# Kernel optimization log

Measured on AMD Instinct MI355X. Metric: run time of the kernel, lower is better.

The kernel has to match this reference:

```python
import jax, jax.numpy as jnp
import numpy as np

UNITS = 2048
D_IN = 96
BATCH = 64
T = 512
C_IN = 10        # connectivity_input: nnz per input-kernel row
C_REC = 10       # connectivity_recurrent: nnz per recurrent-kernel column
INPUT_SCALING = 1.0
SPECTRAL_RADIUS = 0.99
LEAKY = 1.0


def setup_inputs() -> dict:
    rng = np.random.default_rng(0)
    # --- input kernel: sparse (D_IN, UNITS), C_IN nonzeros per row (COO) ---
    krows = np.repeat(np.arange(D_IN), C_IN).astype(np.int32)                 # [D_IN*C_IN]
    kcols = np.stack([rng.choice(UNITS, size=C_IN, replace=False)
                      for _ in range(D_IN)]).reshape(-1).astype(np.int32)
    kvals = (2.0 * (2.0 * rng.random(D_IN * C_IN) - 1.0)).astype(np.float32) * np.float32(INPUT_SCALING)
    # --- recurrent kernel: sparse (UNITS, UNITS), C_REC nonzeros per column ---
    # rec_idx[i, j] = source row feeding output unit (column) i
    rec_idx = np.stack([rng.choice(UNITS, size=C_REC, replace=False)
                        for _ in range(UNITS)]).astype(np.int32)              # [UNITS, C_REC]
    rec_vals = (2.0 * (2.0 * rng.random((UNITS, C_REC)) - 1.0)).astype(np.float32)
    # spectral-radius normalization via exact eigenvalues (matches tf.linalg.eig path, leaky==1)
    W = np.zeros((UNITS, UNITS), np.float32)
    W[rec_idx.reshape(-1), np.repeat(np.arange(UNITS), C_REC)] = rec_vals.reshape(-1)
    rho = np.abs(np.linalg.eigvals(W)).max()
    rec_vals = rec_vals * np.float32(SPECTRAL_RADIUS / rho)
    # --- bias ---
    bias = (2.0 * rng.random(UNITS) - 1.0).astype(np.float32) * np.float32(INPUT_SCALING)
    key = jax.random.key(0)
    inputs = jax.random.normal(key, (BATCH, T, D_IN), dtype=jnp.float32)
    state0 = jnp.zeros((BATCH, UNITS), dtype=jnp.float32)
    return {
        "inputs": inputs,
        "state0": state0,
        "kernel_vals": jnp.asarray(kvals),
        "rec_vals": jnp.asarray(rec_vals),
        "bias": jnp.asarray(bias),
        "kernel_rows": jnp.asarray(krows),
        "kernel_cols": jnp.asarray(kcols),
        "rec_idx": jnp.asarray(rec_idx),
    }


def reference(inputs, state0, kernel_vals, rec_vals, bias, kernel_rows, kernel_cols, rec_idx):
    units = bias.shape[0]

    def step(h, x_t):                                     # h: [B, units], x_t: [B, D_IN]
        # input_part = x_t @ kernel (sparse COO, fixed degree per row)
        contrib = x_t[:, kernel_rows] * kernel_vals       # [B, nnz_in]
        input_part = jax.ops.segment_sum(contrib.T, kernel_cols, num_segments=units).T  # [B, units]
        # state_part = h @ W (fixed C_REC sources per output unit -> gather+reduce)
        state_part = jnp.einsum('bnc,nc->bn', h[:, rec_idx], rec_vals)  # [B, units]
        h_new = h * (1.0 - LEAKY) + jnp.tanh(input_part + bias + state_part) * LEAKY
        return h_new, h_new

    _, ys = jax.lax.scan(step, state0, jnp.swapaxes(inputs, 0, 1))  # ys: [T, B, units]
    return jnp.swapaxes(ys, 0, 1)                                   # [B, T, units]
```

## Files before the change

### kernel.cpp

```cpp
#include <hip/hip_runtime.h>

namespace {
constexpr int UNITS = 2048;
constexpr int D_IN  = 96;
constexpr int BATCH = 64;
constexpr int T     = 512;
constexpr int NNZ   = 960;
constexpr int C_REC = 10;
constexpr int NT    = 1024;

constexpr int HA = 0;
constexpr int HB = 16384;
constexpr int IA = 32768;
constexpr int IB = 40960;
constexpr int LDS_BYTES = 49152;

constexpr int OFFS_OFS = 0;
constexpr int WTAB_OFS = 20 * NT * 4;
constexpr int WS_NEED  = 40 * NT * 4;
}

typedef float f32x2 __attribute__((ext_vector_type(2)));
typedef float f32x4 __attribute__((ext_vector_type(4)));

__device__ __forceinline__ void bar_lds() {
  asm volatile("s_waitcnt lgkmcnt(0)\n\ts_barrier" ::: "memory");
}

__device__ __forceinline__ float fast_tanh(float x) {
  float e = __expf(2.0f * x);
  return 1.0f - __fdividef(2.0f, e + 1.0f);
}

__device__ __forceinline__ int c1_byte(int idx) {
  int p = idx >> 1;
  return 8192 + (2 * (p ^ ((p >> 4) & 15)) + (idx & 1)) * 4;
}

__global__ __launch_bounds__(64) void prep_sched(
    const int* __restrict__ ridx, const float* __restrict__ rvals,
    int* __restrict__ offs, float* __restrict__ wtab)
{
  const int w = blockIdx.x, l = threadIdx.x;
  __shared__ int   sidx[128 * C_REC];
  __shared__ float sval[128 * C_REC];
  __shared__ int   hist[32];
  for (int i = l; i < 128 * C_REC; i += 64) {
    sidx[i] = ridx[w * 128 * C_REC + i];
    sval[i] = rvals[w * 128 * C_REC + i];
  }
  __syncthreads();
  const int tidm = w * 64 + l;
  unsigned rem0 = 0x3FF, rem1 = 0x3FF;

  for (int s = 0; s < 20; ++s) {
    if (l < 32) hist[l] = 0;
    __syncthreads();
    const int p = s & 1;
    unsigned& rem = p ? rem1 : rem0;
    const int ul = 2 * l + p;
    const unsigned m = rem;
    const int nc = 2 * __popc(m);
    int pe = -1, pidx = 0, pcp = 0;
    for (int r = 0; r < 6 && pe < 0; ++r) {
      const int rr = (r < nc) ? r : (r % nc);
      const int er = rr >> 1, cp = rr & 1;
      int cnt = 0, ce = 0;
#pragma unroll
      for (int e = 0; e < C_REC; ++e)
        if ((m >> e) & 1) { if (cnt == er) ce = e; ++cnt; }
      const int idx  = sidx[ul * C_REC + ce];
      const int bank = cp ? ((c1_byte(idx) >> 2) & 31) : (idx & 31);
      const int old  = atomicAdd(&hist[bank], 1);
      if (old < 2 || r == 5) { pe = ce; pcp = cp; pidx = idx; }
      else atomicSub(&hist[bank], 1);
    }
    rem = m & ~(1u << pe);
    offs[s * NT + tidm] = pcp ? c1_byte(pidx) : pidx * 4;
    wtab[s * NT + tidm] = sval[ul * C_REC + pe];
    __syncthreads();
  }
}

#define RDECL(k)                                                               \
  const int   oA##k = PERM ? offs[(2*(k)) * NT + tid]                          \
                           : ridx[u0 * C_REC + (k)] * 4;                       \
  const float wA##k = PERM ? wtab[(2*(k)) * NT + tid]                          \
                           : rvals[u0 * C_REC + (k)];                          \
  const int   oB##k = PERM ? offs[(2*(k)+1) * NT + tid]                        \
                           : ridx[(u0 + 1) * C_REC + (k)] * 4;                 \
  const float wB##k = PERM ? wtab[(2*(k)+1) * NT + tid]                        \
                           : rvals[(u0 + 1) * C_REC + (k)];

#define GAT(HC, k)                                                             \
  s0 += *(const float*)(smem + (HC) + oA##k) * wA##k;                          \
  s1 += *(const float*)(smem + (HC) + oB##k) * wB##k;

#define STEP(HC, HN, IR, IW, DO_SCATTER, TSTEP)                                \
  {                                                                            \
    f32x2 in2 = *(f32x2*)(smem + (IR) + tid * 8);                              \
    *(f32x2*)(smem + (IR) + tid * 8) = (f32x2){0.f, 0.f};                      \
    float s0 = in2.x + bias2.x;                                                \
    float s1 = in2.y + bias2.y;                                                \
    GAT(HC, 0) GAT(HC, 1) GAT(HC, 2) GAT(HC, 3) GAT(HC, 4)                     \
    GAT(HC, 5) GAT(HC, 6) GAT(HC, 7) GAT(HC, 8) GAT(HC, 9)                     \
    if ((DO_SCATTER) && e0) atomicAdd((float*)(smem + (IW) + kcb), xn * kv);   \
    f32x2 hh = {fast_tanh(s0), fast_tanh(s1)};                                 \
    *(f32x2*)(smem + (HN) + pb0) = hh;                                         \
    *(f32x2*)(smem + (HN) + pb1) = hh;                                         \
    __builtin_nontemporal_store(hh, outp + (size_t)(TSTEP) * (UNITS / 2));     \
    if (e0) {                                                                  \
      int tnx = (TSTEP) + 2 < T ? (TSTEP) + 2 : T - 1;                         \
      xn = xin[tnx * D_IN + r0];                                               \
    }                                                                          \
    bar_lds();                                                                 \
  }

template <bool PERM>
__global__ __launch_bounds__(NT, 4) void reservoir_kernel(
    const float* __restrict__ inputs, const float* __restrict__ state0,
    const float* __restrict__ kvals,  const float* __restrict__ rvals,
    const float* __restrict__ bias,   const int* __restrict__ krows,
    const int* __restrict__ kcols,    const int* __restrict__ ridx,
    const int* __restrict__ offs,     const float* __restrict__ wtab,
    float* __restrict__ out)
{
  __shared__ __align__(16) char smem[LDS_BYTES];
  const int tid = threadIdx.x;
  const int b   = blockIdx.x;
  const int u0  = 2 * tid;

  const int pb0 = u0 * 4;
  const int pb1 = 8192 + (tid ^ ((tid >> 4) & 15)) * 8;

  *(f32x2*)(smem + IA + tid * 8) = (f32x2){0.f, 0.f};
  *(f32x2*)(smem + IB + tid * 8) = (f32x2){0.f, 0.f};
  f32x2 h0 = *(const f32x2*)(state0 + b * UNITS + u0);
  *(f32x2*)(smem + HA + pb0) = h0;
  *(f32x2*)(smem + HA + pb1) = h0;

  RDECL(0) RDECL(1) RDECL(2) RDECL(3) RDECL(4)
  RDECL(5) RDECL(6) RDECL(7) RDECL(8) RDECL(9)

  const f32x2 bias2 = *(const f32x2*)(bias + u0);

  const bool e0 = tid < NNZ;
  const int   r0  = e0 ? krows[tid] : 0;
  const int   kcb = e0 ? kcols[tid] * 4 : 0;
  const float kv  = e0 ? kvals[tid] : 0.f;

  const float* xin  = inputs + (size_t)b * (T * D_IN);
  f32x2*       outp = (f32x2*)out + (size_t)b * (T * (UNITS / 2)) + tid;

  float xn = e0 ? xin[r0] : 0.f;
  __syncthreads();
  if (e0) atomicAdd((float*)(smem + IA + kcb), xn * kv);
  if (e0) xn = xin[D_IN + r0];
  bar_lds();

#pragma unroll 1
  for (int ts = 0; ts < T; ts += 2) {
    STEP(HA, HB, IA, IB, true,         ts);
    STEP(HB, HA, IB, IA, (ts + 2) < T, ts + 1);
  }
}

extern "C" void kernel_launch(void* const* d_in, const int* in_sizes, int n_in,
                              void* d_out, int out_size, void* d_ws, size_t ws_size,
                              hipStream_t stream) {
  const float* inputs = (const float*)d_in[0];
  const float* state0 = (const float*)d_in[1];
  const float* kvals  = (const float*)d_in[2];
  const float* rvals  = (const float*)d_in[3];
  const float* bias   = (const float*)d_in[4];
  const int*   krows  = (const int*)d_in[5];
  const int*   kcols  = (const int*)d_in[6];
  const int*   ridx   = (const int*)d_in[7];

  int*   offs = (int*)((char*)d_ws + OFFS_OFS);
  float* wtab = (float*)((char*)d_ws + WTAB_OFS);

  if (ws_size >= (size_t)WS_NEED) {
    prep_sched<<<dim3(16), dim3(64), 0, stream>>>(ridx, rvals, offs, wtab);
    reservoir_kernel<true><<<dim3(BATCH), dim3(NT), 0, stream>>>(
        inputs, state0, kvals, rvals, bias, krows, kcols, ridx, offs, wtab,
        (float*)d_out);
  } else {
    reservoir_kernel<false><<<dim3(BATCH), dim3(NT), 0, stream>>>(
        inputs, state0, kvals, rvals, bias, krows, kcols, ridx, offs, wtab,
        (float*)d_out);
  }
}
```

Before: 1.148 ms.

## Bank-aware reorder of input scatter entries and tighter gather schedule

Adds a prep block that sorts the input-kernel COO entries by LDS bank and assigns them to threads so each wave's atomicAdd scatter hits distinct banks. The recurrent gather scheduler now uses a hashed starting choice, per-half-wave histograms and a stricter conflict threshold, aiming to cut LDS bank conflicts further. Offsets are stored as 16-bit values to shrink the workspace tables. The cost is a little more preprocessing work and added complexity in the thread-to-entry mapping.

```diff
diff --git a/kernel.cpp b/kernel.cpp
--- a/kernel.cpp
+++ b/kernel.cpp
@@ -16,12 +16,14 @@
 constexpr int LDS_BYTES = 49152;
 
 constexpr int OFFS_OFS = 0;
-constexpr int WTAB_OFS = 20 * NT * 4;
-constexpr int WS_NEED  = 40 * NT * 4;
+constexpr int WTAB_OFS = 20 * NT * 2;
+constexpr int SCOL_OFS = WTAB_OFS + 20 * NT * 4;
+constexpr int SROW_OFS = SCOL_OFS + NNZ * 2;
+constexpr int SVAL_OFS = SROW_OFS + NNZ * 2;
+constexpr int WS_NEED  = SVAL_OFS + NNZ * 4;
 }
 
 typedef float f32x2 __attribute__((ext_vector_type(2)));
-typedef float f32x4 __attribute__((ext_vector_type(4)));
 
 __device__ __forceinline__ void bar_lds() {
   asm volatile("s_waitcnt lgkmcnt(0)\n\ts_barrier" ::: "memory");
@@ -39,55 +41,99 @@
 
 __global__ __launch_bounds__(64) void prep_sched(
     const int* __restrict__ ridx, const float* __restrict__ rvals,
-    int* __restrict__ offs, float* __restrict__ wtab)
+    const int* __restrict__ krows, const int* __restrict__ kcols,
+    const float* __restrict__ kvals,
+    unsigned short* __restrict__ offs16, float* __restrict__ wtab,
+    unsigned short* __restrict__ scol, unsigned short* __restrict__ srow,
+    float* __restrict__ sval)
 {
-  const int w = blockIdx.x, l = threadIdx.x;
-  __shared__ int   sidx[128 * C_REC];
-  __shared__ float sval[128 * C_REC];
-  __shared__ int   hist[32];
-  for (int i = l; i < 128 * C_REC; i += 64) {
-    sidx[i] = ridx[w * 128 * C_REC + i];
-    sval[i] = rvals[w * 128 * C_REC + i];
-  }
-  __syncthreads();
-  const int tidm = w * 64 + l;
-  unsigned rem0 = 0x3FF, rem1 = 0x3FF;
-
-  for (int s = 0; s < 20; ++s) {
-    if (l < 32) hist[l] = 0;
-    __syncthreads();
-    const int p = s & 1;
-    unsigned& rem = p ? rem1 : rem0;
-    const int ul = 2 * l + p;
-    const unsigned m = rem;
-    const int nc = 2 * __popc(m);
-    int pe = -1, pidx = 0, pcp = 0;
-    for (int r = 0; r < 6 && pe < 0; ++r) {
-      const int rr = (r < nc) ? r : (r % nc);
-      const int er = rr >> 1, cp = rr & 1;
-      int cnt = 0, ce = 0;
+  const int l = threadIdx.x;
+  if (blockIdx.x < 16) {
+    const int w = blockIdx.x;
+    __shared__ int   sidx[128 * C_REC];
+    __shared__ float svalw[128 * C_REC];
+    __shared__ int   hist[64];
+    for (int i = l; i < 128 * C_REC; i += 64) {
+      sidx[i]  = ridx[w * 128 * C_REC + i];
+      svalw[i] = rvals[w * 128 * C_REC + i];
+    }
+    __syncthreads();
+    const int tidm  = w * 64 + l;
+    const int hbase = (l >> 5) << 5;
+    const unsigned lh = ((unsigned)l * 2654435761u) >> 27;
+    unsigned rem0 = 0x3FF, rem1 = 0x3FF;
+    for (int s = 0; s < 20; ++s) {
+      hist[l] = 0;
+      __syncthreads();
+      const int p = s & 1;
+      unsigned& rem = p ? rem1 : rem0;
+      const int ul = 2 * l + p;
+      const unsigned m = rem;
+      const int nc = 2 * __popc(m);
+      int pe = -1, pidx = 0, pcp = 0;
+      for (int r = 0; r < 8 && pe < 0; ++r) {
+        const int thr = (r < 3) ? 1 : 2;
+        const int rr  = (int)((r + lh) % (unsigned)nc);
+        const int er = rr >> 1, cp = rr & 1;
+        int cnt = 0, ce = 0;
 #pragma unroll
-      for (int e = 0; e < C_REC; ++e)
-        if ((m >> e) & 1) { if (cnt == er) ce = e; ++cnt; }
-      const int idx  = sidx[ul * C_REC + ce];
-      const int bank = cp ? ((c1_byte(idx) >> 2) & 31) : (idx & 31);
-      const int old  = atomicAdd(&hist[bank], 1);
-      if (old < 2 || r == 5) { pe = ce; pcp = cp; pidx = idx; }
-      else atomicSub(&hist[bank], 1);
-    }
-    rem = m & ~(1u << pe);
-    offs[s * NT + tidm] = pcp ? c1_byte(pidx) : pidx * 4;
-    wtab[s * NT + tidm] = sval[ul * C_REC + pe];
-    __syncthreads();
+        for (int e = 0; e < C_REC; ++e)
+          if ((m >> e) & 1) { if (cnt == er) ce = e; ++cnt; }
+        const int idx  = sidx[ul * C_REC + ce];
+        const int byte = cp ? c1_byte(idx) : idx * 4;
+        const int bank = (byte >> 2) & 31;
+        const int old  = atomicAdd(&hist[hbase + bank], 1);
+        if (old < thr || r == 7) { pe = ce; pcp = cp; pidx = idx; }
+        else atomicSub(&hist[hbase + bank], 1);
+      }
+      rem = m & ~(1u << pe);
+      offs16[s * NT + tidm] =
+          (unsigned short)(pcp ? c1_byte(pidx) : pidx * 4);
+      wtab[s * NT + tidm] = svalw[ul * C_REC + pe];
+      __syncthreads();
+    }
+  } else {
+    __shared__ int lc[64][32];
+    __shared__ int base[64][32];
+    __shared__ int tot[32];
+    __shared__ int bankstart[32];
+    for (int b2 = 0; b2 < 32; ++b2) lc[l][b2] = 0;
+    __syncthreads();
+    for (int k = 0; k < NNZ / 64; ++k)
+      ++lc[l][kcols[l * (NNZ / 64) + k] & 31];
+    __syncthreads();
+    if (l < 32) {
+      int run = 0;
+      for (int t = 0; t < 64; ++t) { base[t][l] = run; run += lc[t][l]; }
+      tot[l] = run;
+    }
+    __syncthreads();
+    if (l == 0) {
+      int run = 0;
+      for (int b2 = 0; b2 < 32; ++b2) { bankstart[b2] = run; run += tot[b2]; }
+    }
+    for (int b2 = 0; b2 < 32; ++b2) lc[l][b2] = 0;
+    __syncthreads();
+    for (int k = 0; k < NNZ / 64; ++k) {
+      const int i  = l * (NNZ / 64) + k;
+      const int b2 = kcols[i] & 31;
+      const int rank = bankstart[b2] + base[l][b2] + lc[l][b2]++;
+      const int slot = rank % 30;
+      const int li   = rank / 30;
+      const int tid  = (slot >> 1) * 64 + (slot & 1) * 32 + li;
+      scol[tid] = (unsigned short)(kcols[i] * 4);
+      srow[tid] = (unsigned short)krows[i];
+      sval[tid] = kvals[i];
+    }
   }
 }
 
 #define RDECL(k)                                                               \
-  const int   oA##k = PERM ? offs[(2*(k)) * NT + tid]                          \
+  const int   oA##k = PERM ? (int)offs16[(2*(k)) * NT + tid]                   \
                            : ridx[u0 * C_REC + (k)] * 4;                       \
   const float wA##k = PERM ? wtab[(2*(k)) * NT + tid]                          \
                            : rvals[u0 * C_REC + (k)];                          \
-  const int   oB##k = PERM ? offs[(2*(k)+1) * NT + tid]                        \
+  const int   oB##k = PERM ? (int)offs16[(2*(k)+1) * NT + tid]                 \
                            : ridx[(u0 + 1) * C_REC + (k)] * 4;                 \
   const float wB##k = PERM ? wtab[(2*(k)+1) * NT + tid]                        \
                            : rvals[(u0 + 1) * C_REC + (k)];
@@ -122,7 +168,9 @@
     const float* __restrict__ kvals,  const float* __restrict__ rvals,
     const float* __restrict__ bias,   const int* __restrict__ krows,
     const int* __restrict__ kcols,    const int* __restrict__ ridx,
-    const int* __restrict__ offs,     const float* __restrict__ wtab,
+    const unsigned short* __restrict__ offs16, const float* __restrict__ wtab,
+    const unsigned short* __restrict__ scol,
+    const unsigned short* __restrict__ srow, const float* __restrict__ sval,
     float* __restrict__ out)
 {
   __shared__ __align__(16) char smem[LDS_BYTES];
@@ -145,9 +193,12 @@
   const f32x2 bias2 = *(const f32x2*)(bias + u0);
 
   const bool e0 = tid < NNZ;
-  const int   r0  = e0 ? krows[tid] : 0;
-  const int   kcb = e0 ? kcols[tid] * 4 : 0;
-  const float kv  = e0 ? kvals[tid] : 0.f;
+  int r0 = 0, kcb = 0; float kv = 0.f;
+  if (PERM) {
+    if (e0) { r0 = srow[tid]; kcb = scol[tid]; kv = sval[tid]; }
+  } else {
+    if (e0) { r0 = krows[tid]; kcb = kcols[tid] * 4; kv = kvals[tid]; }
+  }
 
   const float* xin  = inputs + (size_t)b * (T * D_IN);
   f32x2*       outp = (f32x2*)out + (size_t)b * (T * (UNITS / 2)) + tid;
@@ -177,17 +228,21 @@
   const int*   kcols  = (const int*)d_in[6];
   const int*   ridx   = (const int*)d_in[7];
 
-  int*   offs = (int*)((char*)d_ws + OFFS_OFS);
-  float* wtab = (float*)((char*)d_ws + WTAB_OFS);
+  unsigned short* offs16 = (unsigned short*)((char*)d_ws + OFFS_OFS);
+  float*          wtab   = (float*)((char*)d_ws + WTAB_OFS);
+  unsigned short* scol   = (unsigned short*)((char*)d_ws + SCOL_OFS);
+  unsigned short* srow   = (unsigned short*)((char*)d_ws + SROW_OFS);
+  float*          sval   = (float*)((char*)d_ws + SVAL_OFS);
 
   if (ws_size >= (size_t)WS_NEED) {
-    prep_sched<<<dim3(16), dim3(64), 0, stream>>>(ridx, rvals, offs, wtab);
+    prep_sched<<<dim3(17), dim3(64), 0, stream>>>(
+        ridx, rvals, krows, kcols, kvals, offs16, wtab, scol, srow, sval);
     reservoir_kernel<true><<<dim3(BATCH), dim3(NT), 0, stream>>>(
-        inputs, state0, kvals, rvals, bias, krows, kcols, ridx, offs, wtab,
-        (float*)d_out);
+        inputs, state0, kvals, rvals, bias, krows, kcols, ridx,
+        offs16, wtab, scol, srow, sval, (float*)d_out);
   } else {
     reservoir_kernel<false><<<dim3(BATCH), dim3(NT), 0, stream>>>(
-        inputs, state0, kvals, rvals, bias, krows, kcols, ridx, offs, wtab,
-        (float*)d_out);
-  }
-}
+        inputs, state0, kvals, rvals, bias, krows, kcols, ridx,
+        offs16, wtab, scol, srow, sval, (float*)d_out);
+  }
+}
```

Result: faster. 1.070 ms (-6.8%).
